# Kernel optimization log

Measured on AMD Instinct MI355X. Metric: run time of the kernel, lower is better.

Reference implementation:

```python
import jax, jax.numpy as jnp
import numpy as np

N_NODES = 100000
D = 64        # graph_embed_size == utterance_embed_size
B = 64        # batch size == number of groups per layer
K = 500000    # selected candidate nodes per layer
M = 200000    # mention nodes
ATT_H = 20    # attention_hidden_dim
CTX = 4 * D   # context_embed_size = 2*graph + 2*utter


def setup_inputs() -> dict:
    key = jax.random.key(0)
    ks = jax.random.split(key, 16)
    graph_embed = jax.random.normal(ks[0], (N_NODES, D), jnp.float32)
    utterance_embed = jax.random.normal(ks[1], (B, D), jnp.float32)
    mention_index = jax.random.randint(ks[2], (M,), 0, N_NODES)
    mention_batch_index = jnp.sort(jax.random.randint(ks[3], (M,), 0, B))
    sel_indices = jax.random.randint(ks[4], (2, K), 0, N_NODES + 1)
    sel_batch_indices = jnp.sort(jax.random.randint(ks[5], (2, K), 0, B), axis=-1)
    sel_group_indices = jnp.sort(jax.random.randint(ks[6], (2, K), 0, B), axis=-1)
    grp_batch_indices = jnp.tile(jnp.arange(B), (2, 1))  # group i belongs to batch i
    last_indices = jax.random.randint(ks[7], (2, B), 0, N_NODES + 1)
    intent_indices = jax.random.randint(ks[8], (2, B), 0, 3)
    score_masks = jnp.ones((2, K), jnp.float32)
    # learned parameters (torch nn.Linear default init: U(-1/sqrt(fan_in), 1/sqrt(fan_in)))
    s_w = 1.0 / np.sqrt(D)
    s_v = 1.0 / np.sqrt(ATT_H)
    s_c = 1.0 / np.sqrt(CTX)
    att_W = jax.random.uniform(ks[9], (ATT_H, D), jnp.float32, -s_w, s_w)
    att_V = jax.random.uniform(ks[10], (1, ATT_H), jnp.float32, -s_v, s_v)
    W1_w = jax.random.uniform(ks[11], (1, CTX), jnp.float32, -s_c, s_c)
    W1_b = jax.random.uniform(ks[12], (1,), jnp.float32, -s_c, s_c)
    W2_w = jax.random.uniform(ks[13], (1, CTX), jnp.float32, -s_c, s_c)
    W2_b = jax.random.uniform(ks[14], (1,), jnp.float32, -s_c, s_c)
    intent_emb = jax.random.normal(ks[15], (3, D), jnp.float32)
    return dict(graph_embed=graph_embed, utterance_embed=utterance_embed,
                mention_index=mention_index, mention_batch_index=mention_batch_index,
                sel_indices=sel_indices, sel_batch_indices=sel_batch_indices,
                sel_group_indices=sel_group_indices, grp_batch_indices=grp_batch_indices,
                last_indices=last_indices, intent_indices=intent_indices,
                score_masks=score_masks, att_W=att_W, att_V=att_V,
                W1_w=W1_w, W1_b=W1_b, W2_w=W2_w, W2_b=W2_b, intent_emb=intent_emb)


def _segment_attention(embed, batch_index, att_W, att_V):
    # Self_Attention with batch_index: segment softmax + weighted segment sum.
    beta = jnp.squeeze(jnp.tanh(embed @ att_W.T) @ att_V.T, -1)      # [M]
    exp_beta = jnp.exp(beta)                                          # faithful: raw exp
    seg_sum = jax.ops.segment_sum(exp_beta, batch_index, num_segments=B)  # [B]
    alpha = exp_beta / seg_sum[batch_index]                           # [M]
    return jax.ops.segment_sum(alpha[:, None] * embed, batch_index, num_segments=B)  # [B,D]


def _layer(W_w, W_b, utter, portrait, graph_e, sel, sel_b, sel_g, grp_b,
           last, intent, mask, intent_emb, last_weight):
    context = jnp.concatenate([utter, portrait], axis=-1)             # [B,2D]
    feats = graph_e[sel]                                              # [K,D]
    # grp_context = [tiled context | start-point embed | intent embed] -> [G,4D]
    grp_ctx = jnp.concatenate([context[grp_b], graph_e[last], intent_emb[intent]], axis=-1)
    weights = jax.nn.sigmoid(grp_ctx @ W_w.T + W_b)                   # [G,1]
    tu = utter[sel_b]                                                 # [K,D]
    tp = portrait[sel_b]                                              # [K,D]
    w = weights[sel_g]                                                # [K,1]
    scores = jnp.sum((tu * w + tp * (1.0 - w)) * feats, axis=-1)      # [K]
    if last_weight is None:
        return scores, weights
    lw = last_weight[sel_b]                                           # [K,1]
    last_scores = jnp.sum((tu * lw + tp * (1.0 - lw)) * feats, axis=-1)
    return last_scores + mask * scores, None


def reference(graph_embed, utterance_embed, mention_index, mention_batch_index,
              sel_indices, sel_batch_indices, sel_group_indices, grp_batch_indices,
              last_indices, intent_indices, score_masks,
              att_W, att_V, W1_w, W1_b, W2_w, W2_b, intent_emb):
    # user portrait via segment-softmax attention over mentioned nodes
    mention_embed = graph_embed[mention_index]                        # [M,D]
    portrait = _segment_attention(mention_embed, mention_batch_index, att_W, att_V)  # [B,D]
    # extended graph embedding with abstract (zero) row appended
    graph_e = jnp.concatenate([graph_embed, jnp.zeros((1, D), graph_embed.dtype)], axis=0)
    s0, w0 = _layer(W1_w, W1_b, utterance_embed, portrait, graph_e,
                    sel_indices[0], sel_batch_indices[0], sel_group_indices[0],
                    grp_batch_indices[0], last_indices[0], intent_indices[0],
                    score_masks[0], intent_emb, None)
    s1, _ = _layer(W2_w, W2_b, utterance_embed, portrait, graph_e,
                   sel_indices[1], sel_batch_indices[1], sel_group_indices[1],
                   grp_batch_indices[1], last_indices[1], intent_indices[1],
                   score_masks[1], intent_emb, w0)
    return jnp.stack([s0, s1], axis=0)                                # [2,K]
```

## Files before the change

kernel.cpp:

```cpp
#include <hip/hip_runtime.h>
#include <math.h>

#define N_NODES 100000
#define D_EMB   64
#define KSEL    500000
#define NMENT   200000
#define ATT_H   20

#define WS_EB    0
#define WS_NUM   100000
#define WS_DEN   104096
#define WS_PORT  104160
#define WS_W     108256
#define WS_KCODE 108384
#define WS_MCODE 1108384
#define WS_BF_FLOAT_OFF 1308416
#define WS_BF_BYTE ((size_t)WS_BF_FLOAT_OFF * 4)
#define WS_TOTAL_BYTES ((size_t)(WS_BF_FLOAT_OFF + N_NODES * 32) * 4)

#define NPB 391
#define MCB 196
#define KCB 977

__device__ __forceinline__ unsigned pack2bf(float a, float b) {
    unsigned ua = __float_as_uint(a), ub = __float_as_uint(b);
    ua = (ua + 0x7FFFu + ((ua >> 16) & 1u)) >> 16;
    ub = (ub + 0x7FFFu + ((ub >> 16) & 1u)) >> 16;
    return ua | (ub << 16);
}
__device__ __forceinline__ float uasf(unsigned u) { return __uint_as_float(u); }

template<bool PACK>
__global__ __launch_bounds__(256) void kP(const float* __restrict__ ge,
                                          const float* __restrict__ attW,
                                          const float* __restrict__ attV,
                                          const int* __restrict__ mi,
                                          const int* __restrict__ mbi,
                                          const int* __restrict__ sel,
                                          const int* __restrict__ selb,
                                          const int* __restrict__ selg,
                                          float* __restrict__ ws) {
    int bid = blockIdx.x;
    if (PACK && bid >= NPB) {
        int t = threadIdx.x;
        if (bid < NPB + MCB) {
            int base = (bid - NPB) * 1024 + t * 4;
            int* mc = (int*)ws + WS_MCODE;
            if (base + 3 < NMENT) {
                int4 a = *(const int4*)(mi + base);
                int4 b = *(const int4*)(mbi + base);
                int4 o;
                o.x = a.x | (b.x << 17); o.y = a.y | (b.y << 17);
                o.z = a.z | (b.z << 17); o.w = a.w | (b.w << 17);
                *(int4*)(mc + base) = o;
            } else {
                for (int i = base; i < NMENT; ++i) mc[i] = mi[i] | (mbi[i] << 17);
            }
        } else {
            int base = (bid - NPB - MCB) * 1024 + t * 4;
            int* kc = (int*)ws + WS_KCODE;
            if (base + 3 < 2 * KSEL) {
                int4 a = *(const int4*)(sel + base);
                int4 b = *(const int4*)(selb + base);
                int4 g = *(const int4*)(selg + base);
                int4 o;
                o.x = a.x | (b.x << 17) | (g.x << 23);
                o.y = a.y | (b.y << 17) | (g.y << 23);
                o.z = a.z | (b.z << 17) | (g.z << 23);
                o.w = a.w | (b.w << 17) | (g.w << 23);
                *(int4*)(kc + base) = o;
            } else {
                for (int i = base; i < 2 * KSEL; ++i)
                    kc[i] = sel[i] | (selb[i] << 17) | (selg[i] << 23);
            }
        }
        return;
    }

    int tid = bid * 256 + threadIdx.x;
    if (tid < 64 * 64 + 64) ws[WS_NUM + tid] = 0.f;
    if (tid >= N_NODES) return;

    const float4* g4 = (const float4*)(ge + (size_t)tid * D_EMB);
    float4 x[16];
#pragma unroll
    for (int i = 0; i < 16; ++i) x[i] = g4[i];

    if constexpr (PACK) {
        uint4* dst = (uint4*)((char*)ws + WS_BF_BYTE + (size_t)tid * 128);
#pragma unroll
        for (int j = 0; j < 8; ++j) {
            uint4 o;
            o.x = pack2bf(x[2*j].x,   x[2*j].y);
            o.y = pack2bf(x[2*j].z,   x[2*j].w);
            o.z = pack2bf(x[2*j+1].x, x[2*j+1].y);
            o.w = pack2bf(x[2*j+1].z, x[2*j+1].w);
            dst[j] = o;
        }
    }

    float beta = 0.f;
#pragma unroll
    for (int j = 0; j < ATT_H; ++j) {
        float h = 0.f;
#pragma unroll
        for (int i = 0; i < 16; ++i) {
            float4 w = ((const float4*)(attW + j * D_EMB))[i];
            h += w.x * x[i].x + w.y * x[i].y + w.z * x[i].z + w.w * x[i].w;
        }
        beta += attV[j] * tanhf(h);
    }
    ws[WS_EB + tid] = expf(beta);
}

__global__ __launch_bounds__(256, 8) void kA2n(float* __restrict__ ws) {
    __shared__ float lacc[64 * 64];
    __shared__ float lden[64];
    for (int i = threadIdx.x; i < 64 * 64; i += 256) lacc[i] = 0.f;
    if (threadIdx.x < 64) lden[threadIdx.x] = 0.f;
    __syncthreads();

    const int* mc = (const int*)ws + WS_MCODE;
    const unsigned short* bft = (const unsigned short*)((const char*)ws + WS_BF_BYTE);

    int lane = threadIdx.x & 63;
    int grp  = lane >> 4, lp = lane & 15;
    int wave = blockIdx.x * 4 + (threadIdx.x >> 6);
    int s = wave * 25;

    int cd[7]; float ebv[7]; uint2 rr[7];
#pragma unroll
    for (int i = 0; i < 7; ++i) {
        bool v = (4 * i + grp) < 25;
        cd[i] = v ? mc[s + 4 * i + grp] : 0;
    }
#pragma unroll
    for (int i = 0; i < 7; ++i) {
        bool v = (4 * i + grp) < 25;
        int nd = cd[i] & 0x1FFFF;
        ebv[i] = v ? ws[WS_EB + nd] : 0.f;
        rr[i]  = *(const uint2*)(bft + (size_t)nd * 64 + lp * 4);
    }

    int curb = (cd[0] >> 17) & 63;
    float4 acc = make_float4(0.f, 0.f, 0.f, 0.f);
    float dacc = 0.f;
#pragma unroll
    for (int i = 0; i < 7; ++i) {
        int b = (cd[i] >> 17) & 63;
        bool v = (4 * i + grp) < 25;
        if (v && b != curb) {
            atomicAdd(&lacc[curb * 64 + lp * 4 + 0], acc.x);
            atomicAdd(&lacc[curb * 64 + lp * 4 + 1], acc.y);
            atomicAdd(&lacc[curb * 64 + lp * 4 + 2], acc.z);
            atomicAdd(&lacc[curb * 64 + lp * 4 + 3], acc.w);
            if (lp == 0) atomicAdd(&lden[curb], dacc);
            acc = make_float4(0.f, 0.f, 0.f, 0.f); dacc = 0.f; curb = b;
        }
        float e = ebv[i];
        acc.x = fmaf(e, uasf(rr[i].x << 16),         acc.x);
        acc.y = fmaf(e, uasf(rr[i].x & 0xFFFF0000u), acc.y);
        acc.z = fmaf(e, uasf(rr[i].y << 16),         acc.z);
        acc.w = fmaf(e, uasf(rr[i].y & 0xFFFF0000u), acc.w);
        dacc += e;
    }
    atomicAdd(&lacc[curb * 64 + lp * 4 + 0], acc.x);
    atomicAdd(&lacc[curb * 64 + lp * 4 + 1], acc.y);
    atomicAdd(&lacc[curb * 64 + lp * 4 + 2], acc.z);
    atomicAdd(&lacc[curb * 64 + lp * 4 + 3], acc.w);
    if (lp == 0) atomicAdd(&lden[curb], dacc);
    __syncthreads();

    int sB = blockIdx.x * 100;
    int b0 = (mc[sB] >> 17) & 63;
    int b1 = (mc[sB + 99] >> 17) & 63;
    int nb = b1 - b0 + 1;
    for (int idx = threadIdx.x; idx < nb * 64; idx += 256) {
        int bb = b0 + (idx >> 6), d = idx & 63;
        float v = lacc[bb * 64 + d];
        if (v != 0.f) atomicAdd(&ws[WS_NUM + bb * 64 + d], v);
    }
    if (threadIdx.x < nb) {
        float v = lden[b0 + threadIdx.x];
        if (v != 0.f) atomicAdd(&ws[WS_DEN + b0 + threadIdx.x], v);
    }
}

__global__ __launch_bounds__(64) void kBW(const float* __restrict__ ge,
                                          const float* __restrict__ utter,
                                          const int* __restrict__ grpb,
                                          const int* __restrict__ lastI,
                                          const int* __restrict__ intentI,
                                          const float* __restrict__ W1w,
                                          const float* __restrict__ W1b,
                                          const float* __restrict__ W2w,
                                          const float* __restrict__ W2b,
                                          const float* __restrict__ intentEmb,
                                          float* __restrict__ ws) {
    int bi = blockIdx.x;
    int l  = bi >> 6;
    int g  = bi & 63;
    int d  = threadIdx.x;

    if (l == 0) {
        ws[WS_PORT + g * 64 + d] = ws[WS_NUM + g * 64 + d] / ws[WS_DEN + g];
    }
    int gb = grpb[bi];
    float pd = ws[WS_NUM + gb * 64 + d] / ws[WS_DEN + gb];

    int last = lastI[bi];
    float gl = (last < N_NODES) ? ge[(size_t)last * D_EMB + d] : 0.f;
    int it = intentI[bi];
    float ie = intentEmb[it * D_EMB + d];

    const float* Ww = (l == 0) ? W1w : W2w;
    float bias      = (l == 0) ? W1b[0] : W2b[0];

    float val = utter[gb * D_EMB + d] * Ww[d]
              + pd * Ww[64 + d]
              + gl * Ww[128 + d]
              + ie * Ww[192 + d];
#pragma unroll
    for (int off = 32; off; off >>= 1) val += __shfl_xor(val, off);
    if (d == 0) ws[WS_W + bi] = 1.f / (1.f + expf(-(val + bias)));
}

__global__ __launch_bounds__(512, 8) void kCn(const float* __restrict__ utter,
                                              const float* __restrict__ masks,
                                              const float* __restrict__ ws,
                                              float* __restrict__ out) {
    __shared__ float4 sU[64 * 17];
    __shared__ float4 sP[64 * 17];
    __shared__ float  sWd[128];

    for (int i = threadIdx.x; i < 64 * 16; i += 512) {
        int r = i >> 4, c = i & 15;
        sU[r * 17 + c] = ((const float4*)utter)[i];
        sP[r * 17 + c] = ((const float4*)(ws + WS_PORT))[i];
    }
    if (threadIdx.x < 128) sWd[threadIdx.x] = ws[WS_W + threadIdx.x];
    __syncthreads();

    int lane = threadIdx.x & 63;
    int wave = blockIdx.x * 8 + (threadIdx.x >> 6);
    const int W = gridDim.x * 8;
    int grp = lane >> 3;
    int lp  = lane & 7;

    const int* kc = (const int*)ws + WS_KCODE;
    const unsigned short* bft = (const unsigned short*)((const char*)ws + WS_BF_BYTE);
    const int NGRP = 2 * KSEL / 8;
    const int L2G  = KSEL / 8;

#define LDC(GI, CD, MK) { int gi_ = (GI); bool v_ = gi_ < NGRP; int kk_ = gi_ * 8 + grp; \
        CD = v_ ? kc[kk_] : N_NODES; \
        MK = (v_ && gi_ >= L2G) ? masks[kk_] : 0.f; }
#define LDR(CD, R) { int nd_ = (CD) & 0x1FFFF; \
        R = make_uint4(0u, 0u, 0u, 0u); \
        if (nd_ < N_NODES) R = *(const uint4*)(bft + (size_t)nd_ * 64 + lp * 8); }

    int cd0, cd1, cd2, cd3; float mk0, mk1, mk2, mk3;
    uint4 R0, R1, R2;
    LDC(wave,         cd0, mk0);
    LDC(wave + W,     cd1, mk1);
    LDC(wave + 2 * W, cd2, mk2);
    LDR(cd0, R0);
    LDR(cd1, R1);

    for (int gi = wave; gi < NGRP; gi += W) {
        LDR(cd2, R2);
        LDC(gi + 3 * W, cd3, mk3);

        int b = (cd0 >> 17) & 63;
        int g = (cd0 >> 23) & 63;
        float cu, cp;
        if (gi < L2G) {
            float w = sWd[g]; cu = w; cp = 1.f - w;
        } else {
            float lw = sWd[b]; float w1 = sWd[64 + g];
            cu = fmaf(mk0, w1, lw);
            cp = fmaf(mk0, 1.f - w1, 1.f - lw);
        }
        float4 tu0 = sU[b * 17 + 2 * lp], tu1 = sU[b * 17 + 2 * lp + 1];
        float4 tp0 = sP[b * 17 + 2 * lp], tp1 = sP[b * 17 + 2 * lp + 1];
        float f, val;
        f = uasf(R0.x << 16);         val  = (cu * tu0.x + cp * tp0.x) * f;
        f = uasf(R0.x & 0xFFFF0000u); val += (cu * tu0.y + cp * tp0.y) * f;
        f = uasf(R0.y << 16);         val += (cu * tu0.z + cp * tp0.z) * f;
        f = uasf(R0.y & 0xFFFF0000u); val += (cu * tu0.w + cp * tp0.w) * f;
        f = uasf(R0.z << 16);         val += (cu * tu1.x + cp * tp1.x) * f;
        f = uasf(R0.z & 0xFFFF0000u); val += (cu * tu1.y + cp * tp1.y) * f;
        f = uasf(R0.w << 16);         val += (cu * tu1.z + cp * tp1.z) * f;
        f = uasf(R0.w & 0xFFFF0000u); val += (cu * tu1.w + cp * tp1.w) * f;
        val += __shfl_xor(val, 1);
        val += __shfl_xor(val, 2);
        val += __shfl_xor(val, 4);
        if (lp == 0) out[gi * 8 + grp] = val;

        cd0 = cd1; mk0 = mk1; cd1 = cd2; mk1 = mk2; cd2 = cd3; mk2 = mk3;
        R0 = R1; R1 = R2;
    }
#undef LDC
#undef LDR
}

#define KA2_L 25
__global__ __launch_bounds__(256) void kA2_fb(const float* __restrict__ ge,
                                              const int* __restrict__ mi,
                                              const int* __restrict__ mbi,
                                              float* __restrict__ ws) {
    int lane = threadIdx.x & 63;
    int wave = (blockIdx.x * 256 + threadIdx.x) >> 6;
    int wstart = wave * KA2_L;
    if (wstart >= NMENT) return;
    int wend = min(wstart + KA2_L, NMENT);
    int len  = wend - wstart;

    int idx    = wstart + lane;
    bool valid = idx < wend;
    int lastB  = mbi[wend - 1];
    int nd     = valid ? mi[idx] : 0;
    int bb     = valid ? mbi[idx] : lastB;
    float ebv  = valid ? ws[WS_EB + nd] : 0.f;
    int code   = nd | (bb << 17);

    float acc = 0.f, dacc = 0.f;
    int curb = __shfl(code, 0) >> 17;

    int Lr = (len + 3) & ~3;
    for (int u0 = 0; u0 < Lr; u0 += 4) {
        int c4[4]; float e4[4]; float x4[4];
#pragma unroll
        for (int j = 0; j < 4; ++j) {
            int u = u0 + j;
            c4[j] = __shfl(code, u);
            e4[j] = __shfl(ebv, u);
            x4[j] = ge[(size_t)(c4[j] & 0x1FFFF) * D_EMB + lane];
        }
#pragma unroll
        for (int j = 0; j < 4; ++j) {
            int b = c4[j] >> 17;
            if (b != curb) {
                atomicAdd(&ws[WS_NUM + curb * 64 + lane], acc);
                if (lane == 0) atomicAdd(&ws[WS_DEN + curb], dacc);
                acc = 0.f; dacc = 0.f; curb = b;
            }
            acc  = fmaf(e4[j], x4[j], acc);
            dacc += e4[j];
        }
    }
    atomicAdd(&ws[WS_NUM + curb * 64 + lane], acc);
    if (lane == 0) atomicAdd(&ws[WS_DEN + curb], dacc);
}

__global__ __launch_bounds__(512, 8) void kC_fb(const float* __restrict__ ge,
                                                const float* __restrict__ utter,
                                                const int* __restrict__ sel,
                                                const int* __restrict__ selb,
                                                const int* __restrict__ selg,
                                                const float* __restrict__ masks,
                                                const float* __restrict__ ws,
                                                float* __restrict__ out) {
    __shared__ float4 sU[64 * 17];
    __shared__ float4 sP[64 * 17];
    __shared__ float  sW[128];
    for (int i = threadIdx.x; i < 64 * 16; i += 512) {
        int r = i >> 4, c = i & 15;
        sU[r * 17 + c] = ((const float4*)utter)[i];
        sP[r * 17 + c] = ((const float4*)(ws + WS_PORT))[i];
    }
    if (threadIdx.x < 128) sW[threadIdx.x] = ws[WS_W + threadIdx.x];
    __syncthreads();

    int lane = threadIdx.x & 63;
    int wave = blockIdx.x * 8 + (threadIdx.x >> 6);
    int W = gridDim.x * 8;
    int grp = lane >> 4, lp = lane & 15;
    const float4* g4 = (const float4*)ge;
    const int NGRP = 2 * KSEL / 4;

    for (int gi = wave; gi < NGRP; gi += W) {
        int kk = gi * 4 + grp;
        int node = sel[kk], b = selb[kk], g = selg[kk];
        float cu, cp;
        if (kk < KSEL) { float w = sW[g]; cu = w; cp = 1.f - w; }
        else {
            float mask = masks[kk]; float lw = sW[b]; float w1 = sW[64 + g];
            cu = fmaf(mask, w1, lw); cp = fmaf(mask, 1.f - w1, 1.f - lw);
        }
        float4 f = make_float4(0.f, 0.f, 0.f, 0.f);
        if (node < N_NODES) f = g4[(size_t)node * 16 + lp];
        float4 tu = sU[b * 17 + lp];
        float4 tp = sP[b * 17 + lp];
        float val = (cu * tu.x + cp * tp.x) * f.x
                  + (cu * tu.y + cp * tp.y) * f.y
                  + (cu * tu.z + cp * tp.z) * f.z
                  + (cu * tu.w + cp * tp.w) * f.w;
        val += __shfl_xor(val, 1);
        val += __shfl_xor(val, 2);
        val += __shfl_xor(val, 4);
        val += __shfl_xor(val, 8);
        if (lp == 0) out[kk] = val;
    }
}

extern "C" void kernel_launch(void* const* d_in, const int* in_sizes, int n_in,
                              void* d_out, int out_size, void* d_ws, size_t ws_size,
                              hipStream_t stream) {
    const float* ge        = (const float*)d_in[0];
    const float* utter     = (const float*)d_in[1];
    const int*   mi        = (const int*)d_in[2];
    const int*   mbi       = (const int*)d_in[3];
    const int*   sel       = (const int*)d_in[4];
    const int*   selb      = (const int*)d_in[5];
    const int*   selg      = (const int*)d_in[6];
    const int*   grpb      = (const int*)d_in[7];
    const int*   lastI     = (const int*)d_in[8];
    const int*   intentI   = (const int*)d_in[9];
    const float* masks     = (const float*)d_in[10];
    const float* attW      = (const float*)d_in[11];
    const float* attV      = (const float*)d_in[12];
    const float* W1w       = (const float*)d_in[13];
    const float* W1b       = (const float*)d_in[14];
    const float* W2w       = (const float*)d_in[15];
    const float* W2b       = (const float*)d_in[16];
    const float* intentEmb = (const float*)d_in[17];
    float* ws  = (float*)d_ws;
    float* out = (float*)d_out;

    bool full = ws_size >= WS_TOTAL_BYTES;

    if (full) {
        kP<true><<<dim3(NPB + MCB + KCB), dim3(256), 0, stream>>>(
            ge, attW, attV, mi, mbi, sel, selb, selg, ws);
        kA2n<<<dim3(2000), dim3(256), 0, stream>>>(ws);
        kBW<<<dim3(128), dim3(64), 0, stream>>>(ge, utter, grpb, lastI, intentI,
                                                W1w, W1b, W2w, W2b, intentEmb, ws);
        kCn<<<dim3(1024), dim3(512), 0, stream>>>(utter, masks, ws, out);
    } else {
        kP<false><<<dim3(NPB), dim3(256), 0, stream>>>(
            ge, attW, attV, mi, mbi, sel, selb, selg, ws);
        kA2_fb<<<dim3(2000), dim3(256), 0, stream>>>(ge, mi, mbi, ws);
        kBW<<<dim3(128), dim3(64), 0, stream>>>(ge, utter, grpb, lastI, intentI,
                                                W1w, W1b, W2w, W2b, intentEmb, ws);
        kC_fb<<<dim3(1024), dim3(512), 0, stream>>>(ge, utter, sel, selb, selg,
                                                    masks, ws, out);
    }
}
```

Measured before the change: 79.88 us.

## Precompute node-by-batch dot table with MFMA, then score by table lookup

Replaces the per-candidate 64-wide dot-product kernel with two kernels. The first uses bf16 MFMA to compute, for every node, its dot products against all 64 utterance and 64 portrait vectors, and stores them as a packed bf16 pair table laid out batch-major. The second reads one 32-bit table entry per candidate and mixes the two values with the layer weights. This trades 1M gathers of 128-byte rows for a dense 100k×128 GEMM plus 1M 4-byte gathers, at the cost of an extra launch, about 25MB of table writes, and bf16 rounding of the dot results.

```diff
diff --git a/kernel.cpp b/kernel.cpp
--- a/kernel.cpp
+++ b/kernel.cpp
@@ -6,6 +6,7 @@
 #define KSEL    500000
 #define NMENT   200000
 #define ATT_H   20
+#define NPAD    100008
 
 #define WS_EB    0
 #define WS_NUM   100000
@@ -16,11 +17,15 @@
 #define WS_MCODE 1108384
 #define WS_BF_FLOAT_OFF 1308416
 #define WS_BF_BYTE ((size_t)WS_BF_FLOAT_OFF * 4)
-#define WS_TOTAL_BYTES ((size_t)(WS_BF_FLOAT_OFF + N_NODES * 32) * 4)
+#define WS_T     4508416
+#define WS_TOTAL_BYTES ((size_t)(WS_T + 64 * NPAD) * 4)
 
 #define NPB 391
 #define MCB 196
 #define KCB 977
+
+typedef __attribute__((ext_vector_type(8))) short bf16x8;
+typedef __attribute__((ext_vector_type(4))) float f32x4;
 
 __device__ __forceinline__ unsigned pack2bf(float a, float b) {
     unsigned ua = __float_as_uint(a), ub = __float_as_uint(b);
@@ -225,83 +230,108 @@
     if (d == 0) ws[WS_W + bi] = 1.f / (1.f + expf(-(val + bias)));
 }
 
-__global__ __launch_bounds__(512, 8) void kCn(const float* __restrict__ utter,
-                                              const float* __restrict__ masks,
-                                              const float* __restrict__ ws,
-                                              float* __restrict__ out) {
-    __shared__ float4 sU[64 * 17];
-    __shared__ float4 sP[64 * 17];
-    __shared__ float  sWd[128];
-
-    for (int i = threadIdx.x; i < 64 * 16; i += 512) {
-        int r = i >> 4, c = i & 15;
-        sU[r * 17 + c] = ((const float4*)utter)[i];
-        sP[r * 17 + c] = ((const float4*)(ws + WS_PORT))[i];
-    }
+__global__ __launch_bounds__(256) void kG(const float* __restrict__ ge,
+                                          const float* __restrict__ utter,
+                                          float* __restrict__ ws) {
+    __shared__ unsigned sQ[128 * 36];
+    __shared__ unsigned sT[4][16 * 65];
+
+    int tid = threadIdx.x;
+    for (int i = tid; i < 128 * 32; i += 256) {
+        int q = i >> 5, c32 = i & 31;
+        int k2 = c32 * 2;
+        float a, b;
+        if (q < 64) { a = utter[q * 64 + k2];               b = utter[q * 64 + k2 + 1]; }
+        else        { a = ws[WS_PORT + (q - 64) * 64 + k2]; b = ws[WS_PORT + (q - 64) * 64 + k2 + 1]; }
+        sQ[q * 36 + c32] = pack2bf(a, b);
+    }
+    __syncthreads();
+
+    int l = tid & 63, w = tid >> 6;
+    int r16 = l & 15, kb = l >> 4;
+
+    bf16x8 Bf[8][2];
+#pragma unroll
+    for (int c = 0; c < 8; ++c)
+#pragma unroll
+        for (int s = 0; s < 2; ++s) {
+            int q = c * 16 + r16;
+            uint4 u = *(const uint4*)&sQ[q * 36 + s * 16 + kb * 4];
+            Bf[c][s] = __builtin_bit_cast(bf16x8, u);
+        }
+
+    unsigned* Tu = (unsigned*)(ws + WS_T);
+
+#pragma unroll 1
+    for (int t = 0; t < 4; ++t) {
+        int nb0 = blockIdx.x * 256 + t * 64 + w * 16;
+        int node = nb0 + r16;
+        bf16x8 Af[2];
+#pragma unroll
+        for (int s = 0; s < 2; ++s) {
+            uint4 u = make_uint4(0u, 0u, 0u, 0u);
+            if (node < N_NODES) {
+                const float* p = ge + (size_t)node * 64 + s * 32 + kb * 8;
+                float4 p0 = *(const float4*)p;
+                float4 p1 = *(const float4*)(p + 4);
+                u = make_uint4(pack2bf(p0.x, p0.y), pack2bf(p0.z, p0.w),
+                               pack2bf(p1.x, p1.y), pack2bf(p1.z, p1.w));
+            }
+            Af[s] = __builtin_bit_cast(bf16x8, u);
+        }
+
+        f32x4 acc[8];
+#pragma unroll
+        for (int c = 0; c < 8; ++c) acc[c] = (f32x4){0.f, 0.f, 0.f, 0.f};
+#pragma unroll
+        for (int s = 0; s < 2; ++s)
+#pragma unroll
+            for (int c = 0; c < 8; ++c)
+                acc[c] = __builtin_amdgcn_mfma_f32_16x16x32_bf16(Af[s], Bf[c][s], acc[c], 0, 0, 0);
+
+#pragma unroll
+        for (int c = 0; c < 4; ++c)
+#pragma unroll
+            for (int r = 0; r < 4; ++r)
+                sT[w][(kb * 4 + r) * 65 + (c * 16 + r16)] = pack2bf(acc[c][r], acc[c + 4][r]);
+        __syncthreads();
+
+#pragma unroll
+        for (int it = 0; it < 16; ++it) {
+            int idx = it * 64 + l;
+            int b = idx >> 4, nn = idx & 15;
+            int node2 = blockIdx.x * 256 + t * 64 + w * 16 + nn;
+            if (node2 < NPAD)
+                Tu[(size_t)b * NPAD + node2] = sT[w][nn * 65 + b];
+        }
+        __syncthreads();
+    }
+}
+
+__global__ __launch_bounds__(256) void kS(const float* __restrict__ masks,
+                                          const float* __restrict__ ws,
+                                          float* __restrict__ out) {
+    __shared__ float sWd[128];
     if (threadIdx.x < 128) sWd[threadIdx.x] = ws[WS_W + threadIdx.x];
     __syncthreads();
-
-    int lane = threadIdx.x & 63;
-    int wave = blockIdx.x * 8 + (threadIdx.x >> 6);
-    const int W = gridDim.x * 8;
-    int grp = lane >> 3;
-    int lp  = lane & 7;
-
+    int kk = blockIdx.x * 256 + threadIdx.x;
+    if (kk >= 2 * KSEL) return;
     const int* kc = (const int*)ws + WS_KCODE;
-    const unsigned short* bft = (const unsigned short*)((const char*)ws + WS_BF_BYTE);
-    const int NGRP = 2 * KSEL / 8;
-    const int L2G  = KSEL / 8;
-
-#define LDC(GI, CD, MK) { int gi_ = (GI); bool v_ = gi_ < NGRP; int kk_ = gi_ * 8 + grp; \
-        CD = v_ ? kc[kk_] : N_NODES; \
-        MK = (v_ && gi_ >= L2G) ? masks[kk_] : 0.f; }
-#define LDR(CD, R) { int nd_ = (CD) & 0x1FFFF; \
-        R = make_uint4(0u, 0u, 0u, 0u); \
-        if (nd_ < N_NODES) R = *(const uint4*)(bft + (size_t)nd_ * 64 + lp * 8); }
-
-    int cd0, cd1, cd2, cd3; float mk0, mk1, mk2, mk3;
-    uint4 R0, R1, R2;
-    LDC(wave,         cd0, mk0);
-    LDC(wave + W,     cd1, mk1);
-    LDC(wave + 2 * W, cd2, mk2);
-    LDR(cd0, R0);
-    LDR(cd1, R1);
-
-    for (int gi = wave; gi < NGRP; gi += W) {
-        LDR(cd2, R2);
-        LDC(gi + 3 * W, cd3, mk3);
-
-        int b = (cd0 >> 17) & 63;
-        int g = (cd0 >> 23) & 63;
-        float cu, cp;
-        if (gi < L2G) {
-            float w = sWd[g]; cu = w; cp = 1.f - w;
-        } else {
-            float lw = sWd[b]; float w1 = sWd[64 + g];
-            cu = fmaf(mk0, w1, lw);
-            cp = fmaf(mk0, 1.f - w1, 1.f - lw);
-        }
-        float4 tu0 = sU[b * 17 + 2 * lp], tu1 = sU[b * 17 + 2 * lp + 1];
-        float4 tp0 = sP[b * 17 + 2 * lp], tp1 = sP[b * 17 + 2 * lp + 1];
-        float f, val;
-        f = uasf(R0.x << 16);         val  = (cu * tu0.x + cp * tp0.x) * f;
-        f = uasf(R0.x & 0xFFFF0000u); val += (cu * tu0.y + cp * tp0.y) * f;
-        f = uasf(R0.y << 16);         val += (cu * tu0.z + cp * tp0.z) * f;
-        f = uasf(R0.y & 0xFFFF0000u); val += (cu * tu0.w + cp * tp0.w) * f;
-        f = uasf(R0.z << 16);         val += (cu * tu1.x + cp * tp1.x) * f;
-        f = uasf(R0.z & 0xFFFF0000u); val += (cu * tu1.y + cp * tp1.y) * f;
-        f = uasf(R0.w << 16);         val += (cu * tu1.z + cp * tp1.z) * f;
-        f = uasf(R0.w & 0xFFFF0000u); val += (cu * tu1.w + cp * tp1.w) * f;
-        val += __shfl_xor(val, 1);
-        val += __shfl_xor(val, 2);
-        val += __shfl_xor(val, 4);
-        if (lp == 0) out[gi * 8 + grp] = val;
-
-        cd0 = cd1; mk0 = mk1; cd1 = cd2; mk1 = mk2; cd2 = cd3; mk2 = mk3;
-        R0 = R1; R1 = R2;
-    }
-#undef LDC
-#undef LDR
+    int code = kc[kk];
+    int n = code & 0x1FFFF, b = (code >> 17) & 63, g = (code >> 23) & 63;
+    const unsigned* Tu = (const unsigned*)(ws + WS_T);
+    unsigned t = Tu[(size_t)b * NPAD + n];
+    float du = uasf(t << 16), dp = uasf(t & 0xFFFF0000u);
+    float cu, cp;
+    if (kk < KSEL) {
+        float wv = sWd[g]; cu = wv; cp = 1.f - wv;
+    } else {
+        float mk = masks[kk];
+        float lw = sWd[b], w1 = sWd[64 + g];
+        cu = fmaf(mk, w1, lw);
+        cp = fmaf(mk, 1.f - w1, 1.f - lw);
+    }
+    out[kk] = cu * du + cp * dp;
 }
 
 #define KA2_L 25
@@ -436,7 +466,8 @@
         kA2n<<<dim3(2000), dim3(256), 0, stream>>>(ws);
         kBW<<<dim3(128), dim3(64), 0, stream>>>(ge, utter, grpb, lastI, intentI,
                                                 W1w, W1b, W2w, W2b, intentEmb, ws);
-        kCn<<<dim3(1024), dim3(512), 0, stream>>>(utter, masks, ws, out);
+        kG<<<dim3((NPAD + 255) / 256 + 1), dim3(256), 0, stream>>>(ge, utter, ws);
+        kS<<<dim3((2 * KSEL + 255) / 256), dim3(256), 0, stream>>>(masks, ws, out);
     } else {
         kP<false><<<dim3(NPB), dim3(256), 0, stream>>>(
             ge, attW, attV, mi, mbi, sel, selb, selg, ws);
```

New measurement: 92.41 us. 1.16x slower.
